# Kernel optimization log

Hardware: AMD Instinct MI355X
Metric: run time of the kernel (lower is better)

## Reference

```python
import jax, jax.numpy as jnp
import numpy as np

Q = 4          # num_quantizers
K = 2048       # codebook_size
D = 256        # dim
B, N = 8, 8192 # batch, tokens (N % Q == 0)


def l2norm(t, eps=1e-12):
    return t / jnp.maximum(jnp.linalg.norm(t, axis=-1, keepdims=True), eps)


def setup_inputs() -> dict:
    key = jax.random.key(0)
    kx, ke = jax.random.split(key)
    x = jax.random.normal(kx, (B, N, D), dtype=jnp.float32)
    embed = jax.random.normal(ke, (Q, K, D), dtype=jnp.float32)
    return {"x": x, "embed": embed}


def reference(x, embed):
    b, n, d = x.shape
    q = embed.shape[0]
    m = n // q  # tokens per quantizer chunk
    # chunk along token axis (dim=1), as torch.chunk(x, Q, dim=1)
    xc = x.reshape(b, q, m, d).transpose(1, 0, 2, 3)  # [Q, B, M, D]

    def one_vq(xq, eq):
        # xq: [B, M, D], eq: [K, D]
        xn = l2norm(xq)
        en = l2norm(eq)
        dist = jnp.einsum('bmd,kd->bmk', xn, en)   # cosine similarity
        ind = jnp.argmax(dist, axis=-1)            # temp=0 gumbel -> argmax
        quant = eq[ind]                            # F.embedding with raw embed
        return quant, ind

    quant_c, ind_c = jax.vmap(one_vq)(xc, embed)   # [Q,B,M,D], [Q,B,M]
    quantized = quant_c.transpose(1, 0, 2, 3).reshape(b, n, d)
    encoding = ind_c.transpose(1, 0, 2).reshape(b, n)
    # eval mode: loss is sum of Q zero tensors of shape [1]
    vq_loss = jnp.zeros((1,), dtype=x.dtype)
    return quantized, encoding, vq_loss
```

## Files before the change

kernel.cpp:

```cpp
#include <hip/hip_runtime.h>
#include <math.h>

#define Bq 8
#define Nq 8192
#define Dq 256
#define Qq 4
#define Kq 2048
#define Mq (Nq / Qq)
#define TT (Bq * Nq)
#define QUANT_ELEMS ((size_t)TT * Dq)

#define CAP1Q 4096
#define THRESH 3e-4f

#define WS_CNT_OFF    0u
#define WS_LIST_OFF   1024u
#define WS_PSC_OFF    66560u
#define WS_PCD_OFF    590848u
#define WS_ENH_OFF    1115136u
#define WS_ENP_OFF    5309440u

typedef __attribute__((ext_vector_type(8))) _Float16 f16x8;
typedef __attribute__((ext_vector_type(4))) _Float16 f16x4;
typedef __attribute__((ext_vector_type(4))) float    f32x4;

__device__ __forceinline__ void async_load16(const void* g, void* s) {
    __builtin_amdgcn_global_load_lds(
        (const __attribute__((address_space(1))) void*)g,
        (__attribute__((address_space(3))) void*)s, 16, 0, 0);
}

__device__ __forceinline__ float f32_div(float a, float b) {
    return (float)((double)a / (double)b);
}

__device__ __forceinline__ float np_norm_wave(const float* __restrict__ src, int ln) {
#pragma clang fp contract(off)
    float r = 0.0f;
    if (ln < 16) {
        const float* p = src + (ln >> 3) * 128 + (ln & 7);
        #pragma unroll
        for (int m = 0; m < 16; ++m) { float v = p[m * 8]; r = r + v * v; }
    }
    float t = r + __shfl_xor(r, 1, 64);
    t = t + __shfl_xor(t, 2, 64);
    t = t + __shfl_xor(t, 4, 64);
    float b0 = __shfl(t, 0, 64);
    float b1 = __shfl(t, 8, 64);
    float n2 = b0 + b1;
    return fmaxf((float)sqrt((double)n2), 1e-12f);
}

__global__ __launch_bounds__(256) void cvt_kernel(const float* __restrict__ embed,
                                                  char* __restrict__ enh) {
    int row = blockIdx.x * 4 + (threadIdx.x >> 6);
    int ln  = threadIdx.x & 63;
    float4 v = *(const float4*)(embed + (size_t)row * Dq + ln * 4);
    float s = v.x * v.x + v.y * v.y + v.z * v.z + v.w * v.w;
    #pragma unroll
    for (int m = 1; m < 64; m <<= 1) s += __shfl_xor(s, m, 64);
    float sx = 1.0f / fmaxf(sqrtf(s), 1e-12f);
    int q = row >> 11, k = row & 2047, Tb = k >> 5, c = k & 31;
    int g = ln >> 1, h = ln & 1;
    f16x4 o;
    o[0] = (_Float16)(v.x * sx); o[1] = (_Float16)(v.y * sx);
    o[2] = (_Float16)(v.z * sx); o[3] = (_Float16)(v.w * sx);
    char* dst = enh + ((size_t)(q * 64 + Tb)) * 16384 + c * 512 + ((g ^ c) << 4) + h * 8;
    *(f16x4*)dst = o;
}

__global__ __launch_bounds__(256) void enp_kernel(const float* __restrict__ embed,
                                                  float* __restrict__ enp) {
    int row = blockIdx.x * 4 + (threadIdx.x >> 6);
    int ln  = threadIdx.x & 63;
    const float* src = embed + (size_t)row * Dq;
    float nm = np_norm_wave(src, ln);
    float* dst = enp + (size_t)row * Dq;
    #pragma unroll
    for (int e = 0; e < 4; ++e) dst[ln * 4 + e] = f32_div(src[ln * 4 + e], nm);
}

__global__ __launch_bounds__(256) void gemm_kernel(const float* __restrict__ x,
                                                   const float* __restrict__ embed,
                                                   const char* __restrict__ enh,
                                                   float* __restrict__ out,
                                                   int* __restrict__ cnt,
                                                   int* __restrict__ list) {
    __shared__ __align__(16) char es[2][16384];

    const int tid = threadIdx.x;
    const int wv  = tid >> 6;
    const int ln  = tid & 63;
    const int qd  = ln >> 4;
    const int l15 = ln & 15;

    const int bid = blockIdx.x;
    const int q   = bid & 3;
    const int w   = bid >> 2;
    const int t0  = (w >> 4) * Nq + q * Mq + (w & 15) * 128;
    const int t0w = t0 + wv * 32;

    f16x8 ah[2][8];
    #pragma unroll
    for (int mf = 0; mf < 2; ++mf) {
        const float* xr = x + (size_t)(t0w + mf * 16 + l15) * Dq + qd * 8;
        float4 xa[16];
        float s2 = 0.f;
        #pragma unroll
        for (int ch = 0; ch < 8; ++ch) {
            float4 u = *(const float4*)(xr + ch * 32);
            float4 v = *(const float4*)(xr + ch * 32 + 4);
            xa[2 * ch] = u; xa[2 * ch + 1] = v;
            s2 += u.x * u.x + u.y * u.y + u.z * u.z + u.w * u.w;
            s2 += v.x * v.x + v.y * v.y + v.z * v.z + v.w * v.w;
        }
        s2 += __shfl_xor(s2, 16, 64);
        s2 += __shfl_xor(s2, 32, 64);
        float sx = 1.0f / fmaxf(sqrtf(s2), 1e-12f);
        #pragma unroll
        for (int ch = 0; ch < 8; ++ch) {
            float4 u = xa[2 * ch], v = xa[2 * ch + 1];
            f16x8 f;
            f[0] = (_Float16)(u.x * sx); f[1] = (_Float16)(u.y * sx);
            f[2] = (_Float16)(u.z * sx); f[3] = (_Float16)(u.w * sx);
            f[4] = (_Float16)(v.x * sx); f[5] = (_Float16)(v.y * sx);
            f[6] = (_Float16)(v.z * sx); f[7] = (_Float16)(v.w * sx);
            ah[mf][ch] = f;
        }
    }

    float b1[2][4], b2[2][4];
    int   ic[2][4];
    #pragma unroll
    for (int mf = 0; mf < 2; ++mf)
        #pragma unroll
        for (int r = 0; r < 4; ++r) { b1[mf][r] = -2.0f; b2[mf][r] = -2.0f; ic[mf][r] = 0; }

    const char* ebase = enh + ((size_t)q * 64) * 16384;

    #pragma unroll
    for (int i = 0; i < 4; ++i) {
        int off = i * 4096 + wv * 1024 + ln * 16;
        async_load16(ebase + off, es[0] + off);
    }
    __syncthreads();

    for (int T = 0; T < 64; ++T) {
        if (T + 1 < 64) {
            const char* src = ebase + (size_t)(T + 1) * 16384;
            #pragma unroll
            for (int i = 0; i < 4; ++i) {
                int off = i * 4096 + wv * 1024 + ln * 16;
                async_load16(src + off, es[(T + 1) & 1] + off);
            }
        }
        const char* esb = es[T & 1];

        #pragma unroll
        for (int s = 0; s < 2; ++s) {
            const int  c  = s * 16 + l15;
            const char* cb = esb + c * 512;
            f16x8 bfr[8];
            #pragma unroll
            for (int ch = 0; ch < 8; ++ch)
                bfr[ch] = *(const f16x8*)(cb + ((((ch << 2) | qd) ^ c) << 4));

            f32x4 a0 = {0.f, 0.f, 0.f, 0.f};
            f32x4 a1 = {0.f, 0.f, 0.f, 0.f};
            #pragma unroll
            for (int ch = 0; ch < 8; ++ch) {
                a0 = __builtin_amdgcn_mfma_f32_16x16x32_f16(ah[0][ch], bfr[ch], a0, 0, 0, 0);
                a1 = __builtin_amdgcn_mfma_f32_16x16x32_f16(ah[1][ch], bfr[ch], a1, 0, 0, 0);
            }
            const int cg = (T << 5) + (s << 4) + l15;
            #pragma unroll
            for (int r = 0; r < 4; ++r) {
                float s0 = a0[r];
                if (s0 > b1[0][r]) { b2[0][r] = b1[0][r]; b1[0][r] = s0; ic[0][r] = cg; }
                else if (s0 > b2[0][r]) b2[0][r] = s0;
                float s1 = a1[r];
                if (s1 > b1[1][r]) { b2[1][r] = b1[1][r]; b1[1][r] = s1; ic[1][r] = cg; }
                else if (s1 > b2[1][r]) b2[1][r] = s1;
            }
        }
        __syncthreads();
    }

    float fb1[2][4], fb2[2][4];
    int   fic[2][4];
    #pragma unroll
    for (int mf = 0; mf < 2; ++mf)
        #pragma unroll
        for (int r = 0; r < 4; ++r) {
            float v1 = b1[mf][r], v2 = b2[mf][r]; int vi = ic[mf][r];
            #pragma unroll
            for (int m = 1; m < 16; m <<= 1) {
                float o1 = __shfl_xor(v1, m, 64);
                float o2 = __shfl_xor(v2, m, 64);
                int   oi = __shfl_xor(vi, m, 64);
                if (o1 > v1 || (o1 == v1 && oi < vi)) { v2 = fmaxf(v1, o2); v1 = o1; vi = oi; }
                else v2 = fmaxf(v2, o1);
            }
            fb1[mf][r] = v1; fb2[mf][r] = v2; fic[mf][r] = vi;
        }

    if (l15 == 0) {
        #pragma unroll
        for (int mf = 0; mf < 2; ++mf)
            #pragma unroll
            for (int r = 0; r < 4; ++r) {
                int t = t0w + mf * 16 + qd * 4 + r;
                out[QUANT_ELEMS + (size_t)t] = (float)fic[mf][r];
                if (fb1[mf][r] - fb2[mf][r] < THRESH) {
                    int pos = atomicAdd(&cnt[q], 1);
                    if (pos < CAP1Q) list[q * CAP1Q + pos] = t;
                }
            }
    }

    const float* eqf = embed + (size_t)q * Kq * Dq;
    #pragma unroll
    for (int mf = 0; mf < 2; ++mf)
        #pragma unroll
        for (int r = 0; r < 4; ++r)
            #pragma unroll
            for (int g = 0; g < 4; ++g) {
                int code = __shfl(fic[mf][r], g * 16, 64);
                int t = t0w + mf * 16 + g * 4 + r;
                float4 v = *(const float4*)(eqf + (size_t)code * Dq + ln * 4);
                *(float4*)(out + (size_t)t * Dq + ln * 4) = v;
            }

    if (bid == 0 && tid == 0) out[QUANT_ELEMS + TT] = 0.0f;
}

__global__ __launch_bounds__(256) void fix_partial(const float* __restrict__ x,
                                                   const float* __restrict__ enp,
                                                   const int* __restrict__ cnt,
                                                   const int* __restrict__ list,
                                                   float* __restrict__ pscore,
                                                   int* __restrict__ pcode) {
#pragma clang fp contract(off)
    __shared__ float xn[16][Dq];
    __shared__ int   stok[16];
    __shared__ float wp_s[4][16];
    __shared__ int   wp_c[4][16];

    const int tid = threadIdx.x;
    const int wv  = tid >> 6;
    const int ln  = tid & 63;

    int cq[4], nbq[4], total = 0;
    #pragma unroll
    for (int q = 0; q < 4; ++q) {
        int c = cnt[q]; if (c > CAP1Q) c = CAP1Q;
        cq[q] = c; nbq[q] = (c + 15) >> 4; total += nbq[q] * 8;
    }

    for (int j = blockIdx.x; j < total; j += gridDim.x) {
        int rem = j, q = 0;
        while (rem >= nbq[q] * 8) { rem -= nbq[q] * 8; ++q; }
        const int batch = rem >> 3, chunk = rem & 7;

        if (tid < 16) {
            int idx = batch * 16 + tid;
            stok[tid] = list[q * CAP1Q + (idx < cq[q] ? idx : batch * 16)];
        }
        __syncthreads();
        for (int r = 0; r < 4; ++r) {
            int i = wv * 4 + r;
            const float* xr = x + (size_t)stok[i] * Dq;
            float nm = np_norm_wave(xr, ln);
            #pragma unroll
            for (int e = 0; e < 4; ++e)
                xn[i][ln * 4 + e] = f32_div(xr[ln * 4 + e], nm);
        }
        __syncthreads();

        const int c = chunk * 256 + tid;
        const float* er = enp + ((size_t)(q * Kq + c)) * Dq;
        float l0[16], l1[16], l2[16], l3[16];
        #pragma unroll
        for (int i = 0; i < 16; ++i) { l0[i] = 0.f; l1[i] = 0.f; l2[i] = 0.f; l3[i] = 0.f; }

        for (int d = 0; d < Dq; d += 4) {
            float4 e = *(const float4*)(er + d);
            #pragma unroll
            for (int i = 0; i < 16; ++i) {
                float4 xv = *(const float4*)&xn[i][d];
                l0[i] = l0[i] + xv.x * e.x;
                l1[i] = l1[i] + xv.y * e.y;
                l2[i] = l2[i] + xv.z * e.z;
                l3[i] = l3[i] + xv.w * e.w;
            }
        }

        #pragma unroll
        for (int i = 0; i < 16; ++i) {
            float s = (l0[i] + l1[i]) + (l2[i] + l3[i]);
            int bc = c;
            #pragma unroll
            for (int m = 1; m < 64; m <<= 1) {
                float os = __shfl_xor(s, m, 64);
                int   oc = __shfl_xor(bc, m, 64);
                if (os > s || (os == s && oc < bc)) { s = os; bc = oc; }
            }
            if (ln == 0) { wp_s[wv][i] = s; wp_c[wv][i] = bc; }
        }
        __syncthreads();
        if (tid < 16) {
            int idx = batch * 16 + tid;
            if (idx < cq[q]) {
                float s = wp_s[0][tid]; int bc = wp_c[0][tid];
                #pragma unroll
                for (int w2 = 1; w2 < 4; ++w2) {
                    float os = wp_s[w2][tid]; int oc = wp_c[w2][tid];
                    if (os > s || (os == s && oc < bc)) { s = os; bc = oc; }
                }
                int p = q * CAP1Q + idx;
                pscore[p * 8 + chunk] = s;
                pcode[p * 8 + chunk]  = bc;
            }
        }
        __syncthreads();
    }
}

__global__ __launch_bounds__(256) void fix_final(const float* __restrict__ embed,
                                                 const int* __restrict__ cnt,
                                                 const int* __restrict__ list,
                                                 const float* __restrict__ pscore,
                                                 const int* __restrict__ pcode,
                                                 float* __restrict__ out) {
    int cq[4], tot = 0;
    #pragma unroll
    for (int q = 0; q < 4; ++q) {
        int c = cnt[q]; if (c > CAP1Q) c = CAP1Q;
        cq[q] = c; tot += c;
    }
    const int wv = threadIdx.x >> 6, ln = threadIdx.x & 63;

    for (int j = blockIdx.x * 4 + wv; j < tot; j += gridDim.x * 4) {
        int rem = j, q = 0;
        while (rem >= cq[q]) { rem -= cq[q]; ++q; }
        int p = q * CAP1Q + rem;
        int t = list[p];
        int bc = 0;
        if (ln == 0) {
            float bs = pscore[p * 8]; bc = pcode[p * 8];
            #pragma unroll
            for (int ch = 1; ch < 8; ++ch) {
                float s = pscore[p * 8 + ch]; int c2 = pcode[p * 8 + ch];
                if (s > bs || (s == bs && c2 < bc)) { bs = s; bc = c2; }
            }
            out[QUANT_ELEMS + (size_t)t] = (float)bc;
        }
        bc = __shfl(bc, 0, 64);
        const float* er = embed + ((size_t)(q * Kq + bc)) * Dq;
        float4 v = *(const float4*)(er + ln * 4);
        *(float4*)(out + (size_t)t * Dq + ln * 4) = v;
    }
}

extern "C" void kernel_launch(void* const* d_in, const int* in_sizes, int n_in,
                              void* d_out, int out_size, void* d_ws, size_t ws_size,
                              hipStream_t stream) {
    const float* x     = (const float*)d_in[0];
    const float* embed = (const float*)d_in[1];
    float* out = (float*)d_out;
    char*  ws  = (char*)d_ws;
    int*   cnt    = (int*)(ws + WS_CNT_OFF);
    int*   list   = (int*)(ws + WS_LIST_OFF);
    float* pscore = (float*)(ws + WS_PSC_OFF);
    int*   pcode  = (int*)(ws + WS_PCD_OFF);
    char*  enh    = ws + WS_ENH_OFF;
    float* enp    = (float*)(ws + WS_ENP_OFF);

    hipMemsetAsync(cnt, 0, 16, stream);
    cvt_kernel<<<(Qq * Kq) / 4, 256, 0, stream>>>(embed, enh);
    enp_kernel<<<(Qq * Kq) / 4, 256, 0, stream>>>(embed, enp);
    gemm_kernel<<<512, 256, 0, stream>>>(x, embed, enh, out, cnt, list);
    fix_partial<<<1024, 256, 0, stream>>>(x, enp, cnt, list, pscore, pcode);
    fix_final<<<256, 256, 0, stream>>>(embed, cnt, list, pscore, pcode, out);
}
```

Measured before the change: 302.1 us.

## Split codebook search across two blocks and merge top-2 in a separate kernel

The GEMM/argmax kernel now splits each quantizer's 2048 codes into two halves handled by separate blocks, doubling the grid to 1024 blocks for better CU occupancy. Each block writes its per-token top-2 scores and index to a workspace buffer. A new merge kernel combines the halves, writes the indices, queues ambiguous tokens and gathers the quantized rows. It also fuses the two embed prep kernels into one and makes the top-2 update branchless with med3/max. The cost is an extra kernel launch and a round trip of partial results through global memory.

New measurement: 290.1 us. 4.0% less time.

```diff
diff --git a/kernel.cpp b/kernel.cpp
--- a/kernel.cpp
+++ b/kernel.cpp
@@ -19,6 +19,7 @@
 #define WS_PCD_OFF    590848u
 #define WS_ENH_OFF    1115136u
 #define WS_ENP_OFF    5309440u
+#define WS_PART_OFF   13698048u
 
 typedef __attribute__((ext_vector_type(8))) _Float16 f16x8;
 typedef __attribute__((ext_vector_type(4))) _Float16 f16x4;
@@ -51,11 +52,14 @@
     return fmaxf((float)sqrt((double)n2), 1e-12f);
 }
 
-__global__ __launch_bounds__(256) void cvt_kernel(const float* __restrict__ embed,
-                                                  char* __restrict__ enh) {
+__global__ __launch_bounds__(256) void prep_kernel(const float* __restrict__ embed,
+                                                   char* __restrict__ enh,
+                                                   float* __restrict__ enp) {
     int row = blockIdx.x * 4 + (threadIdx.x >> 6);
     int ln  = threadIdx.x & 63;
-    float4 v = *(const float4*)(embed + (size_t)row * Dq + ln * 4);
+    const float* src = embed + (size_t)row * Dq;
+
+    float4 v = *(const float4*)(src + ln * 4);
     float s = v.x * v.x + v.y * v.y + v.z * v.z + v.w * v.w;
     #pragma unroll
     for (int m = 1; m < 64; m <<= 1) s += __shfl_xor(s, m, 64);
@@ -67,25 +71,16 @@
     o[2] = (_Float16)(v.z * sx); o[3] = (_Float16)(v.w * sx);
     char* dst = enh + ((size_t)(q * 64 + Tb)) * 16384 + c * 512 + ((g ^ c) << 4) + h * 8;
     *(f16x4*)dst = o;
-}
-
-__global__ __launch_bounds__(256) void enp_kernel(const float* __restrict__ embed,
-                                                  float* __restrict__ enp) {
-    int row = blockIdx.x * 4 + (threadIdx.x >> 6);
-    int ln  = threadIdx.x & 63;
-    const float* src = embed + (size_t)row * Dq;
+
     float nm = np_norm_wave(src, ln);
-    float* dst = enp + (size_t)row * Dq;
-    #pragma unroll
-    for (int e = 0; e < 4; ++e) dst[ln * 4 + e] = f32_div(src[ln * 4 + e], nm);
+    float* dstp = enp + (size_t)row * Dq;
+    #pragma unroll
+    for (int e = 0; e < 4; ++e) dstp[ln * 4 + e] = f32_div(src[ln * 4 + e], nm);
 }
 
 __global__ __launch_bounds__(256) void gemm_kernel(const float* __restrict__ x,
-                                                   const float* __restrict__ embed,
                                                    const char* __restrict__ enh,
-                                                   float* __restrict__ out,
-                                                   int* __restrict__ cnt,
-                                                   int* __restrict__ list) {
+                                                   float4* __restrict__ part) {
     __shared__ __align__(16) char es[2][16384];
 
     const int tid = threadIdx.x;
@@ -96,7 +91,8 @@
 
     const int bid = blockIdx.x;
     const int q   = bid & 3;
-    const int w   = bid >> 2;
+    const int h   = (bid >> 2) & 1;
+    const int w   = bid >> 3;
     const int t0  = (w >> 4) * Nq + q * Mq + (w & 15) * 128;
     const int t0w = t0 + wv * 32;
 
@@ -136,7 +132,7 @@
         #pragma unroll
         for (int r = 0; r < 4; ++r) { b1[mf][r] = -2.0f; b2[mf][r] = -2.0f; ic[mf][r] = 0; }
 
-    const char* ebase = enh + ((size_t)q * 64) * 16384;
+    const char* ebase = enh + ((size_t)(q * 64 + h * 32)) * 16384;
 
     #pragma unroll
     for (int i = 0; i < 4; ++i) {
@@ -145,8 +141,8 @@
     }
     __syncthreads();
 
-    for (int T = 0; T < 64; ++T) {
-        if (T + 1 < 64) {
+    for (int T = 0; T < 32; ++T) {
+        if (T + 1 < 32) {
             const char* src = ebase + (size_t)(T + 1) * 16384;
             #pragma unroll
             for (int i = 0; i < 4; ++i) {
@@ -172,15 +168,19 @@
                 a0 = __builtin_amdgcn_mfma_f32_16x16x32_f16(ah[0][ch], bfr[ch], a0, 0, 0, 0);
                 a1 = __builtin_amdgcn_mfma_f32_16x16x32_f16(ah[1][ch], bfr[ch], a1, 0, 0, 0);
             }
-            const int cg = (T << 5) + (s << 4) + l15;
+            const int cg = (h << 10) | (T << 5) | (s << 4) | l15;
             #pragma unroll
             for (int r = 0; r < 4; ++r) {
                 float s0 = a0[r];
-                if (s0 > b1[0][r]) { b2[0][r] = b1[0][r]; b1[0][r] = s0; ic[0][r] = cg; }
-                else if (s0 > b2[0][r]) b2[0][r] = s0;
+                bool  g0 = s0 > b1[0][r];
+                b2[0][r] = __builtin_amdgcn_fmed3f(s0, b1[0][r], b2[0][r]);
+                b1[0][r] = fmaxf(b1[0][r], s0);
+                ic[0][r] = g0 ? cg : ic[0][r];
                 float s1 = a1[r];
-                if (s1 > b1[1][r]) { b2[1][r] = b1[1][r]; b1[1][r] = s1; ic[1][r] = cg; }
-                else if (s1 > b2[1][r]) b2[1][r] = s1;
+                bool  g1 = s1 > b1[1][r];
+                b2[1][r] = __builtin_amdgcn_fmed3f(s1, b1[1][r], b2[1][r]);
+                b1[1][r] = fmaxf(b1[1][r], s1);
+                ic[1][r] = g1 ? cg : ic[1][r];
             }
         }
         __syncthreads();
@@ -210,28 +210,44 @@
             #pragma unroll
             for (int r = 0; r < 4; ++r) {
                 int t = t0w + mf * 16 + qd * 4 + r;
-                out[QUANT_ELEMS + (size_t)t] = (float)fic[mf][r];
-                if (fb1[mf][r] - fb2[mf][r] < THRESH) {
-                    int pos = atomicAdd(&cnt[q], 1);
-                    if (pos < CAP1Q) list[q * CAP1Q + pos] = t;
-                }
-            }
-    }
-
-    const float* eqf = embed + (size_t)q * Kq * Dq;
-    #pragma unroll
-    for (int mf = 0; mf < 2; ++mf)
-        #pragma unroll
-        for (int r = 0; r < 4; ++r)
-            #pragma unroll
-            for (int g = 0; g < 4; ++g) {
-                int code = __shfl(fic[mf][r], g * 16, 64);
-                int t = t0w + mf * 16 + g * 4 + r;
-                float4 v = *(const float4*)(eqf + (size_t)code * Dq + ln * 4);
-                *(float4*)(out + (size_t)t * Dq + ln * 4) = v;
-            }
-
-    if (bid == 0 && tid == 0) out[QUANT_ELEMS + TT] = 0.0f;
+                float4 pv;
+                pv.x = fb1[mf][r];
+                pv.y = fb2[mf][r];
+                pv.z = __int_as_float(fic[mf][r]);
+                pv.w = 0.f;
+                part[(size_t)h * TT + t] = pv;
+            }
+    }
+}
+
+__global__ __launch_bounds__(256) void merge_kernel(const float* __restrict__ embed,
+                                                    const float4* __restrict__ part,
+                                                    float* __restrict__ out,
+                                                    int* __restrict__ cnt,
+                                                    int* __restrict__ list) {
+    const int wv = threadIdx.x >> 6, ln = threadIdx.x & 63;
+    const int nw = gridDim.x * 4;
+
+    for (int t = blockIdx.x * 4 + wv; t < TT; t += nw) {
+        float4 pa = part[t];
+        float4 pb = part[TT + t];
+        float v1, v2; int vi;
+        if (pb.x > pa.x) { v1 = pb.x; vi = __float_as_int(pb.z); v2 = fmaxf(pa.x, pb.y); }
+        else             { v1 = pa.x; vi = __float_as_int(pa.z); v2 = fmaxf(pb.x, pa.y); }
+        const int q = (t >> 11) & 3;
+
+        if (ln == 0) {
+            out[QUANT_ELEMS + (size_t)t] = (float)vi;
+            if (v1 - v2 < THRESH) {
+                int pos = atomicAdd(&cnt[q], 1);
+                if (pos < CAP1Q) list[q * CAP1Q + pos] = t;
+            }
+        }
+        const float* er = embed + ((size_t)(q * Kq + vi)) * Dq;
+        float4 v = *(const float4*)(er + ln * 4);
+        *(float4*)(out + (size_t)t * Dq + ln * 4) = v;
+    }
+    if (blockIdx.x == 0 && threadIdx.x == 0) out[QUANT_ELEMS + TT] = 0.0f;
 }
 
 __global__ __launch_bounds__(256) void fix_partial(const float* __restrict__ x,
@@ -369,17 +385,18 @@
     const float* embed = (const float*)d_in[1];
     float* out = (float*)d_out;
     char*  ws  = (char*)d_ws;
-    int*   cnt    = (int*)(ws + WS_CNT_OFF);
-    int*   list   = (int*)(ws + WS_LIST_OFF);
-    float* pscore = (float*)(ws + WS_PSC_OFF);
-    int*   pcode  = (int*)(ws + WS_PCD_OFF);
-    char*  enh    = ws + WS_ENH_OFF;
-    float* enp    = (float*)(ws + WS_ENP_OFF);
+    int*    cnt    = (int*)(ws + WS_CNT_OFF);
+    int*    list   = (int*)(ws + WS_LIST_OFF);
+    float*  pscore = (float*)(ws + WS_PSC_OFF);
+    int*    pcode  = (int*)(ws + WS_PCD_OFF);
+    char*   enh    = ws + WS_ENH_OFF;
+    float*  enp    = (float*)(ws + WS_ENP_OFF);
+    float4* part   = (float4*)(ws + WS_PART_OFF);
 
     hipMemsetAsync(cnt, 0, 16, stream);
-    cvt_kernel<<<(Qq * Kq) / 4, 256, 0, stream>>>(embed, enh);
-    enp_kernel<<<(Qq * Kq) / 4, 256, 0, stream>>>(embed, enp);
-    gemm_kernel<<<512, 256, 0, stream>>>(x, embed, enh, out, cnt, list);
+    prep_kernel<<<(Qq * Kq) / 4, 256, 0, stream>>>(embed, enh, enp);
+    gemm_kernel<<<1024, 256, 0, stream>>>(x, enh, part);
+    merge_kernel<<<2048, 256, 0, stream>>>(embed, part, out, cnt, list);
     fix_partial<<<1024, 256, 0, stream>>>(x, enp, cnt, list, pscore, pcode);
     fix_final<<<256, 256, 0, stream>>>(embed, cnt, list, pscore, pcode, out);
 }
```
